# Performance work log

Measured on AMD Instinct MI355X. Metric: run time of the kernel, lower is better.

The kernel has to match this reference:

```python
import jax, jax.numpy as jnp
import numpy as np

HIDDEN = 32  # hard-coded in EdgeModel's Sequential

def setup_inputs() -> dict:
    key = jax.random.key(0)
    ks = jax.random.split(key, 9)
    E, FN, FE, OUT = 200000, 512, 256, 128
    IN = FN + FN + FE  # 1280
    src = jax.random.normal(ks[0], (E, FN), dtype=jnp.float32)
    dest = jax.random.normal(ks[1], (E, FN), dtype=jnp.float32)
    edge_attr = jax.random.normal(ks[2], (E, FE), dtype=jnp.float32)
    u = jax.random.normal(ks[3], (64, 128), dtype=jnp.float32)
    batch = jax.random.randint(ks[4], (E,), 0, 64, dtype=jnp.int64)
    # Linear params, PyTorch default init scale ~ 1/sqrt(fan_in)
    s1 = 1.0 / np.sqrt(IN)
    s2 = 1.0 / np.sqrt(HIDDEN)
    W1 = jax.random.uniform(ks[5], (IN, HIDDEN), jnp.float32, -s1, s1)
    b1 = jax.random.uniform(ks[6], (HIDDEN,), jnp.float32, -s1, s1)
    W2 = jax.random.uniform(ks[7], (HIDDEN, OUT), jnp.float32, -s2, s2)
    b2 = jax.random.uniform(ks[8], (OUT,), jnp.float32, -s2, s2)
    return {"src": src, "dest": dest, "edge_attr": edge_attr, "u": u,
            "batch": batch, "W1": W1, "b1": b1, "W2": W2, "b2": b2}

def reference(src, dest, edge_attr, u, batch, W1, b1, W2, b2):
    # concat along feature dim, then Linear -> ELU -> Linear (u, batch unused)
    x = jnp.concatenate([src, dest, edge_attr], axis=1)  # [E, 2*FN+FE]
    h = jax.nn.elu(x @ W1 + b1)                           # [E, 32]
    return h @ W2 + b2                                    # [E, OUT]
```

## Files before the change

### kernel.cpp

```cpp
#include <hip/hip_runtime.h>
#include <hip/hip_bf16.h>

typedef __bf16 bf16x8 __attribute__((ext_vector_type(8)));
typedef unsigned short u16x8 __attribute__((ext_vector_type(8)));
typedef float f32x4 __attribute__((ext_vector_type(4)));
typedef unsigned int u32x4 __attribute__((ext_vector_type(4)));

__global__ __launch_bounds__(256) void prep_w_kernel(
    const float* __restrict__ W1, const float* __restrict__ W2,
    unsigned short* __restrict__ wsB1, unsigned short* __restrict__ wsB2) {
  int tid = blockIdx.x * 256 + threadIdx.x;
  if (tid < 40960) {
    int j = tid & 7, l = (tid >> 3) & 63, nt = (tid >> 9) & 1, kt = tid >> 10;
    int k = kt * 32 + ((l >> 4) << 3) + j;
    int n = nt * 16 + (l & 15);
    __bf16 v = (__bf16)W1[k * 32 + n];
    wsB1[tid] = __builtin_bit_cast(unsigned short, v);
  } else if (tid < 45056) {
    int t = tid - 40960;
    int j = t & 7, l = (t >> 3) & 63, nt = t >> 9;
    int k = ((l >> 4) << 3) + j;
    int n = nt * 16 + (l & 15);
    __bf16 v = (__bf16)W2[k * 128 + n];
    wsB2[t] = __builtin_bit_cast(unsigned short, v);
  }
}

__device__ __forceinline__ u32x4 make_srd(const void* p, unsigned bytes) {
  u32x4 r;
  r[0] = (unsigned)(unsigned long long)p;
  r[1] = (unsigned)(((unsigned long long)p) >> 32);
  r[2] = bytes;
  r[3] = 0x00020000u;
  return r;
}

#define XLD(SLOT, VOFF, OFF0, OFF1)                                        \
  asm volatile("buffer_load_dwordx4 %0, %2, %3, 0 offen offset:" #OFF0     \
               "\n\tbuffer_load_dwordx4 %1, %2, %3, 0 offen offset:" #OFF1 \
               : "=&v"(px[SLOT][0]), "=&v"(px[SLOT][1])                    \
               : "v"(VOFF), "s"(srdX))
#define WLD(SLOT, SOFF)                                                    \
  asm volatile("buffer_load_dwordx4 %0, %2, %3, %4 offen offset:0"         \
               "\n\tbuffer_load_dwordx4 %1, %2, %3, %4 offen offset:1024"  \
               : "=&v"(pw[SLOT][0]), "=&v"(pw[SLOT][1])                    \
               : "v"(voffw), "s"(srdw), "s"((unsigned)(SOFF)))
#define VMW(N)                                                \
  do {                                                        \
    asm volatile("s_waitcnt vmcnt(" #N ")" ::: "memory");     \
    __builtin_amdgcn_sched_barrier(0);                        \
  } while (0)
#define CONS(SX, SW)                                                          \
  do {                                                                        \
    f32x4 lo = px[SX][0], hi = px[SX][1];                                     \
    bf16x8 a;                                                                 \
    a[0] = (__bf16)lo[0]; a[1] = (__bf16)lo[1];                               \
    a[2] = (__bf16)lo[2]; a[3] = (__bf16)lo[3];                               \
    a[4] = (__bf16)hi[0]; a[5] = (__bf16)hi[1];                               \
    a[6] = (__bf16)hi[2]; a[7] = (__bf16)hi[3];                               \
    acc0 = __builtin_amdgcn_mfma_f32_16x16x32_bf16(                           \
        a, __builtin_bit_cast(bf16x8, pw[SW][0]), acc0, 0, 0, 0);             \
    acc1 = __builtin_amdgcn_mfma_f32_16x16x32_bf16(                           \
        a, __builtin_bit_cast(bf16x8, pw[SW][1]), acc1, 0, 0, 0);             \
  } while (0)

template <bool USE_WS>
__global__ __launch_bounds__(256, 4) void edge_mlp_kernel(
    const float* __restrict__ src, const float* __restrict__ dst,
    const float* __restrict__ ea, const float* __restrict__ W1,
    const float* __restrict__ b1, const float* __restrict__ W2,
    const float* __restrict__ b2, const unsigned short* __restrict__ wsB1,
    const unsigned short* __restrict__ wsB2, float* __restrict__ out, int nE) {
  __shared__ alignas(16) unsigned short hbuf_s[4][16 * 40];
  const int lane = threadIdx.x & 63;
  const int wave = threadIdx.x >> 6;
  const int l15 = lane & 15;
  const int lh = lane >> 4;
  const long strip = (long)blockIdx.x * 4 + wave;
  const long e0 = strip * 16;
  if (e0 >= nE) return;
  long row = e0 + l15;
  if (row >= nE) row = nE - 1;

  f32x4 acc0 = {0.f, 0.f, 0.f, 0.f};
  f32x4 acc1 = {0.f, 0.f, 0.f, 0.f};

  if constexpr (USE_WS) {
    const u32x4 srdS = make_srd(src, (unsigned)nE * 2048u);
    const u32x4 srdD = make_srd(dst, (unsigned)nE * 2048u);
    const u32x4 srdE = make_srd(ea, (unsigned)nE * 1024u);
    const u32x4 srdw = make_srd(wsB1, 81920u);
    const unsigned voffx = (unsigned)row * 2048u + (unsigned)lh * 32u;
    const unsigned voffe = (unsigned)row * 1024u + (unsigned)lh * 32u;
    const unsigned voffw = (unsigned)lane * 16u;

    f32x4 px[6][2];
    u16x8 pw[4][2];

    {
      const u32x4 srdX = srdS;
      XLD(0, voffx, 0, 16);       WLD(0, 0);
      XLD(1, voffx, 128, 144);    WLD(1, 2048);
      XLD(2, voffx, 256, 272);    WLD(2, 4096);
      XLD(3, voffx, 384, 400);    WLD(3, 6144);
      XLD(4, voffx, 512, 528);
      XLD(5, voffx, 640, 656);

      VMW(16); CONS(0, 0); XLD(0, voffx, 768, 784);    WLD(0, 8192);
      VMW(16); CONS(1, 1); XLD(1, voffx, 896, 912);    WLD(1, 10240);
      VMW(16); CONS(2, 2); XLD(2, voffx, 1024, 1040);  WLD(2, 12288);
      VMW(16); CONS(3, 3); XLD(3, voffx, 1152, 1168);  WLD(3, 14336);
      VMW(12); CONS(4, 0); XLD(4, voffx, 1280, 1296);  WLD(0, 16384);
      VMW(12); CONS(5, 1); XLD(5, voffx, 1408, 1424);  WLD(1, 18432);
      VMW(12); CONS(0, 2); XLD(0, voffx, 1536, 1552);  WLD(2, 20480);
      VMW(12); CONS(1, 3); XLD(1, voffx, 1664, 1680);  WLD(3, 22528);
      VMW(12); CONS(2, 0); XLD(2, voffx, 1792, 1808);  WLD(0, 24576);
      VMW(12); CONS(3, 1); XLD(3, voffx, 1920, 1936);  WLD(1, 26624);
    }
    {
      const u32x4 srdX = srdD;
      VMW(12); CONS(4, 2); XLD(4, voffx, 0, 16);       WLD(2, 28672);
      VMW(12); CONS(5, 3); XLD(5, voffx, 128, 144);    WLD(3, 30720);
      VMW(12); CONS(0, 0); XLD(0, voffx, 256, 272);    WLD(0, 32768);
      VMW(12); CONS(1, 1); XLD(1, voffx, 384, 400);    WLD(1, 34816);
      VMW(12); CONS(2, 2); XLD(2, voffx, 512, 528);    WLD(2, 36864);
      VMW(12); CONS(3, 3); XLD(3, voffx, 640, 656);    WLD(3, 38912);
      VMW(12); CONS(4, 0); XLD(4, voffx, 768, 784);    WLD(0, 40960);
      VMW(12); CONS(5, 1); XLD(5, voffx, 896, 912);    WLD(1, 43008);
      VMW(12); CONS(0, 2); XLD(0, voffx, 1024, 1040);  WLD(2, 45056);
      VMW(12); CONS(1, 3); XLD(1, voffx, 1152, 1168);  WLD(3, 47104);
      VMW(12); CONS(2, 0); XLD(2, voffx, 1280, 1296);  WLD(0, 49152);
      VMW(12); CONS(3, 1); XLD(3, voffx, 1408, 1424);  WLD(1, 51200);
      VMW(12); CONS(4, 2); XLD(4, voffx, 1536, 1552);  WLD(2, 53248);
      VMW(12); CONS(5, 3); XLD(5, voffx, 1664, 1680);  WLD(3, 55296);
      VMW(12); CONS(0, 0); XLD(0, voffx, 1792, 1808);  WLD(0, 57344);
      VMW(12); CONS(1, 1); XLD(1, voffx, 1920, 1936);  WLD(1, 59392);
    }
    {
      const u32x4 srdX = srdE;
      VMW(12); CONS(2, 2); XLD(2, voffe, 0, 16);       WLD(2, 61440);
      VMW(12); CONS(3, 3); XLD(3, voffe, 128, 144);    WLD(3, 63488);
      VMW(12); CONS(4, 0); XLD(4, voffe, 256, 272);    WLD(0, 65536);
      VMW(12); CONS(5, 1); XLD(5, voffe, 384, 400);    WLD(1, 67584);
      VMW(12); CONS(0, 2); XLD(0, voffe, 512, 528);    WLD(2, 69632);
      VMW(12); CONS(1, 3); XLD(1, voffe, 640, 656);    WLD(3, 71680);
      VMW(12); CONS(2, 0); XLD(2, voffe, 768, 784);    WLD(0, 73728);
      VMW(12); CONS(3, 1); XLD(3, voffe, 896, 912);    WLD(1, 75776);
      VMW(12); CONS(4, 2);                             WLD(2, 77824);
      VMW(10); CONS(5, 3);                             WLD(3, 79872);
      VMW(8);  CONS(0, 0);
      VMW(4);  CONS(1, 1);
      VMW(2);  CONS(2, 2);
      VMW(0);  CONS(3, 3);
    }
  } else {
    for (int t = 0; t < 40; ++t) {
      const float* p = (t < 16) ? (src + row * 512 + t * 32 + lh * 8)
                     : (t < 32) ? (dst + row * 512 + (t - 16) * 32 + lh * 8)
                                : (ea + row * 256 + (t - 32) * 32 + lh * 8);
      f32x4 lo = *(const f32x4*)p;
      f32x4 hi = *(const f32x4*)(p + 4);
      bf16x8 a, bf0, bf1;
      a[0] = (__bf16)lo[0]; a[1] = (__bf16)lo[1];
      a[2] = (__bf16)lo[2]; a[3] = (__bf16)lo[3];
      a[4] = (__bf16)hi[0]; a[5] = (__bf16)hi[1];
      a[6] = (__bf16)hi[2]; a[7] = (__bf16)hi[3];
#pragma unroll
      for (int j = 0; j < 8; ++j) {
        int k = t * 32 + lh * 8 + j;
        bf0[j] = (__bf16)W1[k * 32 + l15];
        bf1[j] = (__bf16)W1[k * 32 + 16 + l15];
      }
      acc0 = __builtin_amdgcn_mfma_f32_16x16x32_bf16(a, bf0, acc0, 0, 0, 0);
      acc1 = __builtin_amdgcn_mfma_f32_16x16x32_bf16(a, bf1, acc1, 0, 0, 0);
    }
  }

  const float bias0 = b1[l15];
  const float bias1 = b1[16 + l15];
  unsigned short* hl = hbuf_s[wave];
#pragma unroll
  for (int r = 0; r < 4; ++r) {
    int hrow = lh * 4 + r;
    float h0 = acc0[r] + bias0;
    float h1 = acc1[r] + bias1;
    h0 = h0 > 0.f ? h0 : (__expf(h0) - 1.f);
    h1 = h1 > 0.f ? h1 : (__expf(h1) - 1.f);
    __bf16 v0 = (__bf16)h0, v1 = (__bf16)h1;
    hl[hrow * 40 + l15] = __builtin_bit_cast(unsigned short, v0);
    hl[hrow * 40 + 16 + l15] = __builtin_bit_cast(unsigned short, v1);
  }
  asm volatile("s_waitcnt lgkmcnt(0)" ::: "memory");
  __builtin_amdgcn_sched_barrier(0);
  bf16x8 ha =
      __builtin_bit_cast(bf16x8, *(const u16x8*)(hl + l15 * 40 + lh * 8));

  f32x4 o[8];
#pragma unroll
  for (int nt = 0; nt < 8; ++nt) {
    bf16x8 bw;
    if (USE_WS) {
      bw = __builtin_bit_cast(bf16x8, *(const u16x8*)(wsB2 + nt * 512 + lane * 8));
    } else {
#pragma unroll
      for (int j = 0; j < 8; ++j)
        bw[j] = (__bf16)W2[(lh * 8 + j) * 128 + nt * 16 + l15];
    }
    f32x4 z = {0.f, 0.f, 0.f, 0.f};
    o[nt] = __builtin_amdgcn_mfma_f32_16x16x32_bf16(ha, bw, z, 0, 0, 0);
  }

#pragma unroll
  for (int nt = 0; nt < 8; ++nt) {
    float bb = b2[nt * 16 + l15];
#pragma unroll
    for (int r = 0; r < 4; ++r) {
      long e = e0 + lh * 4 + r;
      if (e < nE) out[e * 128 + nt * 16 + l15] = o[nt][r] + bb;
    }
  }
}

extern "C" void kernel_launch(void* const* d_in, const int* in_sizes, int n_in,
                              void* d_out, int out_size, void* d_ws,
                              size_t ws_size, hipStream_t stream) {
  const float* src = (const float*)d_in[0];
  const float* dst = (const float*)d_in[1];
  const float* ea = (const float*)d_in[2];
  const float* W1 = (const float*)d_in[5];
  const float* b1 = (const float*)d_in[6];
  const float* W2 = (const float*)d_in[7];
  const float* b2 = (const float*)d_in[8];
  float* out = (float*)d_out;

  const int nE = in_sizes[0] / 512;
  const long strips = (nE + 15) / 16;
  const int nblocks = (int)((strips + 3) / 4);

  unsigned short* wsB1 = (unsigned short*)d_ws;
  unsigned short* wsB2 = wsB1 + 40960;
  const bool use_ws = ws_size >= 45056 * sizeof(unsigned short);

  if (use_ws) {
    prep_w_kernel<<<176, 256, 0, stream>>>(W1, W2, wsB1, wsB2);
    edge_mlp_kernel<true><<<nblocks, 256, 0, stream>>>(
        src, dst, ea, W1, b1, W2, b2, wsB1, wsB2, out, nE);
  } else {
    edge_mlp_kernel<false><<<nblocks, 256, 0, stream>>>(
        src, dst, ea, W1, b1, W2, b2, nullptr, nullptr, out, nE);
  }
}
```

Before: 247.4 us.

## Stream activation tiles through LDS via global_load_lds instead of VGPR buffer loads

Replaces the register-staged buffer loads of the src/dest/edge_attr rows with direct global-to-LDS loads into a per-wave six-slot ring, then reads each slot back with ds_read_b128 before the bf16 conversion and MFMA. The intent is to cut VGPR pressure from the 12 in-flight f32x4 prefetch registers and let the memory system write straight to LDS. In exchange it adds an LDS round trip with a full lgkmcnt wait per step. The ring takes 48KB of LDS per block, and the occupancy hint drops from 4 to 3 blocks per CU. The hidden-layer buffer now reuses the ring memory, and the bias loads move ahead of the main loop.

After: 252.4 us. +2.0%, slower.

```diff
diff --git a/kernel.cpp b/kernel.cpp
--- a/kernel.cpp
+++ b/kernel.cpp
@@ -5,6 +5,9 @@
 typedef unsigned short u16x8 __attribute__((ext_vector_type(8)));
 typedef float f32x4 __attribute__((ext_vector_type(4)));
 typedef unsigned int u32x4 __attribute__((ext_vector_type(4)));
+
+using gptr_t = const __attribute__((address_space(1))) unsigned int*;
+using lptr_t = __attribute__((address_space(3))) unsigned int*;
 
 __global__ __launch_bounds__(256) void prep_w_kernel(
     const float* __restrict__ W1, const float* __restrict__ W2,
@@ -35,16 +38,21 @@
   return r;
 }
 
-#define XLD(SLOT, VOFF, OFF0, OFF1)                                        \
-  asm volatile("buffer_load_dwordx4 %0, %2, %3, 0 offen offset:" #OFF0     \
-               "\n\tbuffer_load_dwordx4 %1, %2, %3, 0 offen offset:" #OFF1 \
-               : "=&v"(px[SLOT][0]), "=&v"(px[SLOT][1])                    \
-               : "v"(VOFF), "s"(srdX))
+#define XLDS(SLOT, GP, FOFF)                                                   \
+  do {                                                                         \
+    __builtin_amdgcn_global_load_lds((gptr_t)(const void*)((GP) + (FOFF)),     \
+                                     (lptr_t)(void*)(ringw + (SLOT) * 512),    \
+                                     16, 0, 0);                                \
+    __builtin_amdgcn_global_load_lds((gptr_t)(const void*)((GP) + (FOFF) + 4), \
+                                     (lptr_t)(void*)(ringw + (SLOT) * 512 + 256), \
+                                     16, 0, 0);                                \
+  } while (0)
 #define WLD(SLOT, SOFF)                                                    \
   asm volatile("buffer_load_dwordx4 %0, %2, %3, %4 offen offset:0"         \
                "\n\tbuffer_load_dwordx4 %1, %2, %3, %4 offen offset:1024"  \
                : "=&v"(pw[SLOT][0]), "=&v"(pw[SLOT][1])                    \
-               : "v"(voffw), "s"(srdw), "s"((unsigned)(SOFF)))
+               : "v"(voffw), "s"(srdw), "s"((unsigned)(SOFF))              \
+               : "memory")
 #define VMW(N)                                                \
   do {                                                        \
     asm volatile("s_waitcnt vmcnt(" #N ")" ::: "memory");     \
@@ -52,7 +60,14 @@
   } while (0)
 #define CONS(SX, SW)                                                          \
   do {                                                                        \
-    f32x4 lo = px[SX][0], hi = px[SX][1];                                     \
+    f32x4 lo, hi;                                                             \
+    asm volatile("ds_read_b128 %0, %2\n\t"                                    \
+                 "ds_read_b128 %1, %2 offset:1024\n\t"                        \
+                 "s_waitcnt lgkmcnt(0)"                                       \
+                 : "=&v"(lo), "=&v"(hi)                                       \
+                 : "v"(ldsrd + (SX) * 2048u)                                  \
+                 : "memory");                                                 \
+    __builtin_amdgcn_sched_barrier(0);                                        \
     bf16x8 a;                                                                 \
     a[0] = (__bf16)lo[0]; a[1] = (__bf16)lo[1];                               \
     a[2] = (__bf16)lo[2]; a[3] = (__bf16)lo[3];                               \
@@ -65,13 +80,13 @@
   } while (0)
 
 template <bool USE_WS>
-__global__ __launch_bounds__(256, 4) void edge_mlp_kernel(
+__global__ __launch_bounds__(256, 3) void edge_mlp_kernel(
     const float* __restrict__ src, const float* __restrict__ dst,
     const float* __restrict__ ea, const float* __restrict__ W1,
     const float* __restrict__ b1, const float* __restrict__ W2,
     const float* __restrict__ b2, const unsigned short* __restrict__ wsB1,
     const unsigned short* __restrict__ wsB2, float* __restrict__ out, int nE) {
-  __shared__ alignas(16) unsigned short hbuf_s[4][16 * 40];
+  __shared__ alignas(16) float ring_s[4][6][512];
   const int lane = threadIdx.x & 63;
   const int wave = threadIdx.x >> 6;
   const int l15 = lane & 15;
@@ -82,77 +97,72 @@
   long row = e0 + l15;
   if (row >= nE) row = nE - 1;
 
+  float* ringw = &ring_s[wave][0][0];
+  const float bias0 = b1[l15];
+  const float bias1 = b1[16 + l15];
+
   f32x4 acc0 = {0.f, 0.f, 0.f, 0.f};
   f32x4 acc1 = {0.f, 0.f, 0.f, 0.f};
 
   if constexpr (USE_WS) {
-    const u32x4 srdS = make_srd(src, (unsigned)nE * 2048u);
-    const u32x4 srdD = make_srd(dst, (unsigned)nE * 2048u);
-    const u32x4 srdE = make_srd(ea, (unsigned)nE * 1024u);
     const u32x4 srdw = make_srd(wsB1, 81920u);
-    const unsigned voffx = (unsigned)row * 2048u + (unsigned)lh * 32u;
-    const unsigned voffe = (unsigned)row * 1024u + (unsigned)lh * 32u;
     const unsigned voffw = (unsigned)lane * 16u;
-
-    f32x4 px[6][2];
+    const float* psrc = src + row * 512 + lh * 8;
+    const float* pdst = dst + row * 512 + lh * 8;
+    const float* pea = ea + row * 256 + lh * 8;
+    const unsigned ldsrd =
+        (unsigned)(unsigned long long)(__attribute__((address_space(3))) void*)
+            ringw + (unsigned)lane * 16u;
+
     u16x8 pw[4][2];
 
-    {
-      const u32x4 srdX = srdS;
-      XLD(0, voffx, 0, 16);       WLD(0, 0);
-      XLD(1, voffx, 128, 144);    WLD(1, 2048);
-      XLD(2, voffx, 256, 272);    WLD(2, 4096);
-      XLD(3, voffx, 384, 400);    WLD(3, 6144);
-      XLD(4, voffx, 512, 528);
-      XLD(5, voffx, 640, 656);
-
-      VMW(16); CONS(0, 0); XLD(0, voffx, 768, 784);    WLD(0, 8192);
-      VMW(16); CONS(1, 1); XLD(1, voffx, 896, 912);    WLD(1, 10240);
-      VMW(16); CONS(2, 2); XLD(2, voffx, 1024, 1040);  WLD(2, 12288);
-      VMW(16); CONS(3, 3); XLD(3, voffx, 1152, 1168);  WLD(3, 14336);
-      VMW(12); CONS(4, 0); XLD(4, voffx, 1280, 1296);  WLD(0, 16384);
-      VMW(12); CONS(5, 1); XLD(5, voffx, 1408, 1424);  WLD(1, 18432);
-      VMW(12); CONS(0, 2); XLD(0, voffx, 1536, 1552);  WLD(2, 20480);
-      VMW(12); CONS(1, 3); XLD(1, voffx, 1664, 1680);  WLD(3, 22528);
-      VMW(12); CONS(2, 0); XLD(2, voffx, 1792, 1808);  WLD(0, 24576);
-      VMW(12); CONS(3, 1); XLD(3, voffx, 1920, 1936);  WLD(1, 26624);
-    }
-    {
-      const u32x4 srdX = srdD;
-      VMW(12); CONS(4, 2); XLD(4, voffx, 0, 16);       WLD(2, 28672);
-      VMW(12); CONS(5, 3); XLD(5, voffx, 128, 144);    WLD(3, 30720);
-      VMW(12); CONS(0, 0); XLD(0, voffx, 256, 272);    WLD(0, 32768);
-      VMW(12); CONS(1, 1); XLD(1, voffx, 384, 400);    WLD(1, 34816);
-      VMW(12); CONS(2, 2); XLD(2, voffx, 512, 528);    WLD(2, 36864);
-      VMW(12); CONS(3, 3); XLD(3, voffx, 640, 656);    WLD(3, 38912);
-      VMW(12); CONS(4, 0); XLD(4, voffx, 768, 784);    WLD(0, 40960);
-      VMW(12); CONS(5, 1); XLD(5, voffx, 896, 912);    WLD(1, 43008);
-      VMW(12); CONS(0, 2); XLD(0, voffx, 1024, 1040);  WLD(2, 45056);
-      VMW(12); CONS(1, 3); XLD(1, voffx, 1152, 1168);  WLD(3, 47104);
-      VMW(12); CONS(2, 0); XLD(2, voffx, 1280, 1296);  WLD(0, 49152);
-      VMW(12); CONS(3, 1); XLD(3, voffx, 1408, 1424);  WLD(1, 51200);
-      VMW(12); CONS(4, 2); XLD(4, voffx, 1536, 1552);  WLD(2, 53248);
-      VMW(12); CONS(5, 3); XLD(5, voffx, 1664, 1680);  WLD(3, 55296);
-      VMW(12); CONS(0, 0); XLD(0, voffx, 1792, 1808);  WLD(0, 57344);
-      VMW(12); CONS(1, 1); XLD(1, voffx, 1920, 1936);  WLD(1, 59392);
-    }
-    {
-      const u32x4 srdX = srdE;
-      VMW(12); CONS(2, 2); XLD(2, voffe, 0, 16);       WLD(2, 61440);
-      VMW(12); CONS(3, 3); XLD(3, voffe, 128, 144);    WLD(3, 63488);
-      VMW(12); CONS(4, 0); XLD(4, voffe, 256, 272);    WLD(0, 65536);
-      VMW(12); CONS(5, 1); XLD(5, voffe, 384, 400);    WLD(1, 67584);
-      VMW(12); CONS(0, 2); XLD(0, voffe, 512, 528);    WLD(2, 69632);
-      VMW(12); CONS(1, 3); XLD(1, voffe, 640, 656);    WLD(3, 71680);
-      VMW(12); CONS(2, 0); XLD(2, voffe, 768, 784);    WLD(0, 73728);
-      VMW(12); CONS(3, 1); XLD(3, voffe, 896, 912);    WLD(1, 75776);
-      VMW(12); CONS(4, 2);                             WLD(2, 77824);
-      VMW(10); CONS(5, 3);                             WLD(3, 79872);
-      VMW(8);  CONS(0, 0);
-      VMW(4);  CONS(1, 1);
-      VMW(2);  CONS(2, 2);
-      VMW(0);  CONS(3, 3);
-    }
+    XLDS(0, psrc, 0);    WLD(0, 0);
+    XLDS(1, psrc, 32);   WLD(1, 2048);
+    XLDS(2, psrc, 64);   WLD(2, 4096);
+    XLDS(3, psrc, 96);   WLD(3, 6144);
+    XLDS(4, psrc, 128);
+    XLDS(5, psrc, 160);
+
+    VMW(16); CONS(0, 0); XLDS(0, psrc, 192); WLD(0, 8192);
+    VMW(16); CONS(1, 1); XLDS(1, psrc, 224); WLD(1, 10240);
+    VMW(16); CONS(2, 2); XLDS(2, psrc, 256); WLD(2, 12288);
+    VMW(16); CONS(3, 3); XLDS(3, psrc, 288); WLD(3, 14336);
+    VMW(12); CONS(4, 0); XLDS(4, psrc, 320); WLD(0, 16384);
+    VMW(12); CONS(5, 1); XLDS(5, psrc, 352); WLD(1, 18432);
+    VMW(12); CONS(0, 2); XLDS(0, psrc, 384); WLD(2, 20480);
+    VMW(12); CONS(1, 3); XLDS(1, psrc, 416); WLD(3, 22528);
+    VMW(12); CONS(2, 0); XLDS(2, psrc, 448); WLD(0, 24576);
+    VMW(12); CONS(3, 1); XLDS(3, psrc, 480); WLD(1, 26624);
+    VMW(12); CONS(4, 2); XLDS(4, pdst, 0);   WLD(2, 28672);
+    VMW(12); CONS(5, 3); XLDS(5, pdst, 32);  WLD(3, 30720);
+    VMW(12); CONS(0, 0); XLDS(0, pdst, 64);  WLD(0, 32768);
+    VMW(12); CONS(1, 1); XLDS(1, pdst, 96);  WLD(1, 34816);
+    VMW(12); CONS(2, 2); XLDS(2, pdst, 128); WLD(2, 36864);
+    VMW(12); CONS(3, 3); XLDS(3, pdst, 160); WLD(3, 38912);
+    VMW(12); CONS(4, 0); XLDS(4, pdst, 192); WLD(0, 40960);
+    VMW(12); CONS(5, 1); XLDS(5, pdst, 224); WLD(1, 43008);
+    VMW(12); CONS(0, 2); XLDS(0, pdst, 256); WLD(2, 45056);
+    VMW(12); CONS(1, 3); XLDS(1, pdst, 288); WLD(3, 47104);
+    VMW(12); CONS(2, 0); XLDS(2, pdst, 320); WLD(0, 49152);
+    VMW(12); CONS(3, 1); XLDS(3, pdst, 352); WLD(1, 51200);
+    VMW(12); CONS(4, 2); XLDS(4, pdst, 384); WLD(2, 53248);
+    VMW(12); CONS(5, 3); XLDS(5, pdst, 416); WLD(3, 55296);
+    VMW(12); CONS(0, 0); XLDS(0, pdst, 448); WLD(0, 57344);
+    VMW(12); CONS(1, 1); XLDS(1, pdst, 480); WLD(1, 59392);
+    VMW(12); CONS(2, 2); XLDS(2, pea, 0);    WLD(2, 61440);
+    VMW(12); CONS(3, 3); XLDS(3, pea, 32);   WLD(3, 63488);
+    VMW(12); CONS(4, 0); XLDS(4, pea, 64);   WLD(0, 65536);
+    VMW(12); CONS(5, 1); XLDS(5, pea, 96);   WLD(1, 67584);
+    VMW(12); CONS(0, 2); XLDS(0, pea, 128);  WLD(2, 69632);
+    VMW(12); CONS(1, 3); XLDS(1, pea, 160);  WLD(3, 71680);
+    VMW(12); CONS(2, 0); XLDS(2, pea, 192);  WLD(0, 73728);
+    VMW(12); CONS(3, 1); XLDS(3, pea, 224);  WLD(1, 75776);
+    VMW(12); CONS(4, 2);                     WLD(2, 77824);
+    VMW(10); CONS(5, 3);                     WLD(3, 79872);
+    VMW(8);  CONS(0, 0);
+    VMW(4);  CONS(1, 1);
+    VMW(2);  CONS(2, 2);
+    VMW(0);  CONS(3, 3);
   } else {
     for (int t = 0; t < 40; ++t) {
       const float* p = (t < 16) ? (src + row * 512 + t * 32 + lh * 8)
@@ -176,9 +186,7 @@
     }
   }
 
-  const float bias0 = b1[l15];
-  const float bias1 = b1[16 + l15];
-  unsigned short* hl = hbuf_s[wave];
+  unsigned short* hl = (unsigned short*)ringw;
 #pragma unroll
   for (int r = 0; r < 4; ++r) {
     int hrow = lh * 4 + r;
```
